# Kernel optimization log

Measured on AMD Instinct MI355X. Metric: run time of the kernel, lower is better.

The kernel has to match this reference:

```python
import jax, jax.numpy as jnp
import numpy as np
import math

N_EMBD = 1024
N_HEAD = 16
HEAD_DIM = N_EMBD // N_HEAD
SCALE = 1.0 / math.sqrt(HEAD_DIM)


def setup_inputs() -> dict:
    key = jax.random.key(0)
    ks = jax.random.split(key, 5)
    B, S = 1, 4096
    std = 0.02
    x = jax.random.normal(ks[0], (B, S, N_EMBD), dtype=jnp.float32)
    # Linear weights stored as [in, out] (transposed vs torch storage; same math)
    w_qkv = jax.random.normal(ks[1], (N_EMBD, 3 * N_EMBD), dtype=jnp.float32) * std
    b_qkv = jnp.zeros((3 * N_EMBD,), dtype=jnp.float32)
    w_out = jax.random.normal(ks[2], (N_EMBD, N_EMBD), dtype=jnp.float32) * std
    b_out = jnp.zeros((N_EMBD,), dtype=jnp.float32)
    return {"x": x, "w_qkv": w_qkv, "b_qkv": b_qkv, "w_out": w_out, "b_out": b_out}


def reference(x, w_qkv, b_qkv, w_out, b_out):
    B, S, D = x.shape
    qkv = x @ w_qkv + b_qkv                      # [B, S, 3D]
    q, k, v = jnp.split(qkv, 3, axis=-1)
    # [B, H, S, d]
    q = q.reshape(B, S, N_HEAD, HEAD_DIM).transpose(0, 2, 1, 3)
    k = k.reshape(B, S, N_HEAD, HEAD_DIM).transpose(0, 2, 1, 3)
    v = v.reshape(B, S, N_HEAD, HEAD_DIM).transpose(0, 2, 1, 3)
    scores = jnp.einsum("bhqd,bhkd->bhqk", q, k) * SCALE  # [B, H, S, S]
    causal = jnp.tril(jnp.ones((S, S), dtype=bool))
    scores = jnp.where(causal, scores, -jnp.inf)
    attn = jax.nn.softmax(scores, axis=-1)
    out = jnp.einsum("bhqk,bhkd->bhqd", attn, v)  # [B, H, S, d]
    out = out.transpose(0, 2, 1, 3).reshape(B, S, D)
    return out @ w_out + b_out
```

## Files before the change

### kernel.cpp

```cpp
#include <hip/hip_runtime.h>
#include <hip/hip_bf16.h>
#include <cstdint>

typedef __bf16 bf16x8 __attribute__((ext_vector_type(8)));
typedef float  f32x4  __attribute__((ext_vector_type(4)));

#define S_LEN 4096
#define D_EMB 1024
#define N3    3072
#define HDIM  64

__device__ __forceinline__ unsigned short f2bf(float f) {
    union { unsigned int i; float f; } v; v.f = f;
    unsigned int i = v.i;
    return (unsigned short)((i + 0x7FFFu + ((i >> 16) & 1u)) >> 16);
}

__device__ __forceinline__ void async16(const void* g, void* l) {
    __builtin_amdgcn_global_load_lds(
        (const __attribute__((address_space(1))) unsigned int*)g,
        (__attribute__((address_space(3))) unsigned int*)l,
        16, 0, 0);
}

__global__ void convert_f32_bf16(const float* __restrict__ src,
                                 unsigned short* __restrict__ dst, int n8) {
    const int i = blockIdx.x * blockDim.x + threadIdx.x;
    if (i >= n8) return;
    float4 f0 = *(const float4*)&src[i * 8];
    float4 f1 = *(const float4*)&src[i * 8 + 4];
    union { uint4 q; unsigned short s[8]; } o;
    o.s[0]=f2bf(f0.x); o.s[1]=f2bf(f0.y); o.s[2]=f2bf(f0.z); o.s[3]=f2bf(f0.w);
    o.s[4]=f2bf(f1.x); o.s[5]=f2bf(f1.y); o.s[6]=f2bf(f1.z); o.s[7]=f2bf(f1.w);
    *(uint4*)&dst[i * 8] = o.q;
}

__global__ void transpose_f32_to_bf16(const float* __restrict__ src,
                                      unsigned short* __restrict__ dst,
                                      int R, int ld, int c0) {
    __shared__ float tile[32][33];
    const int tx = threadIdx.x, ty = threadIdx.y;
    const int r0 = blockIdx.y * 32, cc0 = blockIdx.x * 32;
    for (int i = 0; i < 32; i += 8)
        tile[ty + i][tx] = src[(size_t)(r0 + ty + i) * ld + c0 + cc0 + tx];
    __syncthreads();
    for (int i = 0; i < 32; i += 8)
        dst[(size_t)(cc0 + ty + i) * R + r0 + tx] = f2bf(tile[tx][ty + i]);
}

__global__ void transpose_bf16(const unsigned short* __restrict__ src,
                               unsigned short* __restrict__ dst,
                               int R, int ld, int c0) {
    __shared__ unsigned short tile[32][33];
    const int tx = threadIdx.x, ty = threadIdx.y;
    const int r0 = blockIdx.y * 32, cc0 = blockIdx.x * 32;
    for (int i = 0; i < 32; i += 8)
        tile[ty + i][tx] = src[(size_t)(r0 + ty + i) * ld + c0 + cc0 + tx];
    __syncthreads();
    for (int i = 0; i < 32; i += 8)
        dst[(size_t)(cc0 + ty + i) * R + r0 + tx] = tile[tx][ty + i];
}

template <bool OUT_F32>
__global__ __launch_bounds__(256) void gemm_bt_bias(
    const unsigned short* __restrict__ A,
    const unsigned short* __restrict__ BT,
    const float* __restrict__ bias,
    void* __restrict__ Cp,
    int M, int N, int K)
{
    __shared__ __align__(16) unsigned short As[128 * 32];
    __shared__ __align__(16) unsigned short Bs[128 * 32];
    const int tid  = threadIdx.x;
    const int wave = tid >> 6, lane = tid & 63;
    const int q4 = lane >> 4, l16 = lane & 15;
    const int m0 = blockIdx.y * 128, n0 = blockIdx.x * 128;
    const int wm = (wave >> 1) * 64, wn = (wave & 1) * 64;

    f32x4 acc[4][4] = {};

    const int srow = wave * 32 + (lane >> 2);
    const int scol = (lane & 3) * 8;

    for (int k0 = 0; k0 < K; k0 += 32) {
        __syncthreads();
        for (int i = 0; i < 2; ++i) {
            const int r = srow + i * 16;
            async16(A  + (size_t)(m0 + r) * K + k0 + scol,
                    &As[(wave * 32 + i * 16) * 32 + lane * 8]);
            async16(BT + (size_t)(n0 + r) * K + k0 + scol,
                    &Bs[(wave * 32 + i * 16) * 32 + lane * 8]);
        }
        __syncthreads();

        bf16x8 af[4], bfr[4];
        for (int mi = 0; mi < 4; ++mi)
            af[mi] = *(const bf16x8*)&As[(wm + mi * 16 + l16) * 32 + q4 * 8];
        for (int ni = 0; ni < 4; ++ni)
            bfr[ni] = *(const bf16x8*)&Bs[(wn + ni * 16 + l16) * 32 + q4 * 8];
        for (int mi = 0; mi < 4; ++mi)
            for (int ni = 0; ni < 4; ++ni)
                acc[mi][ni] = __builtin_amdgcn_mfma_f32_16x16x32_bf16(
                    af[mi], bfr[ni], acc[mi][ni], 0, 0, 0);
    }

    for (int ni = 0; ni < 4; ++ni) {
        const int col = n0 + wn + ni * 16 + l16;
        const float bv = bias[col];
        for (int mi = 0; mi < 4; ++mi) {
            const int row = m0 + wm + mi * 16 + q4 * 4;
            for (int r = 0; r < 4; ++r) {
                const float val = acc[mi][ni][r] + bv;
                if constexpr (OUT_F32)
                    ((float*)Cp)[(size_t)(row + r) * N + col] = val;
                else
                    ((unsigned short*)Cp)[(size_t)(row + r) * N + col] = f2bf(val);
            }
        }
    }
}

#define LDP 72
__global__ __launch_bounds__(256) void attn_flash(
    const unsigned short* __restrict__ qkv,
    const unsigned short* __restrict__ Vt,
    unsigned short* __restrict__ X2)
{
    __shared__ __align__(16) unsigned short Ks[64 * LDP];
    __shared__ __align__(16) unsigned short Vs[64 * LDP];
    __shared__ __align__(16) unsigned short Ps[4 * 16 * LDP];
    const int tid  = threadIdx.x;
    const int wave = tid >> 6, lane = tid & 63;
    const int q4 = lane >> 4, l16 = lane & 15;
    const int h  = blockIdx.y;

    const int x = blockIdx.x, hg = blockIdx.y >> 2;
    int qt;
    if      (hg == 0) qt = x;
    else if (hg == 1) qt = 63 - x;
    else if (hg == 2) qt = (x + 16) & 63;
    else              qt = (47 - x) & 63;
    const int q0 = qt * 64;

    bf16x8 aq[2];
    {
        const unsigned short* qp =
            qkv + (size_t)(q0 + wave * 16 + l16) * N3 + h * HDIM + q4 * 8;
        aq[0] = *(const bf16x8*)(qp);
        aq[1] = *(const bf16x8*)(qp + 32);
    }

    float l_part[4] = {0.f, 0.f, 0.f, 0.f};
    f32x4 o[4] = {};

    const int rr = tid >> 3;
    const int cc = (tid & 7) * 8;
    const int ntile = qt + 1;

    for (int t = 0; t < ntile; ++t) {
        const int kv0 = t * 64;
        uint4 kv_a = *(const uint4*)&qkv[(size_t)(kv0 + rr)      * N3 + D_EMB + h * HDIM + cc];
        uint4 kv_b = *(const uint4*)&qkv[(size_t)(kv0 + 32 + rr) * N3 + D_EMB + h * HDIM + cc];
        uint4 vt_a = *(const uint4*)&Vt [(size_t)(h * HDIM + rr)      * S_LEN + kv0 + cc];
        uint4 vt_b = *(const uint4*)&Vt [(size_t)(h * HDIM + 32 + rr) * S_LEN + kv0 + cc];
        __syncthreads();
        *(uint4*)&Ks[rr * LDP + cc]        = kv_a;
        *(uint4*)&Ks[(32 + rr) * LDP + cc] = kv_b;
        *(uint4*)&Vs[rr * LDP + cc]        = vt_a;
        *(uint4*)&Vs[(32 + rr) * LDP + cc] = vt_b;
        __syncthreads();

        f32x4 sacc[4] = {};
        for (int kk = 0; kk < 2; ++kk)
            for (int nt = 0; nt < 4; ++nt) {
                bf16x8 b = *(const bf16x8*)&Ks[(nt * 16 + l16) * LDP + kk * 32 + q4 * 8];
                sacc[nt] = __builtin_amdgcn_mfma_f32_16x16x32_bf16(
                    aq[kk], b, sacc[nt], 0, 0, 0);
            }

        const bool lastt = (t == ntile - 1);
        for (int r = 0; r < 4; ++r) {
            const int grow = q0 + wave * 16 + q4 * 4 + r;
            for (int nt = 0; nt < 4; ++nt) {
                float e = __expf(sacc[nt][r] * 0.125f);
                if (lastt && (kv0 + nt * 16 + l16 > grow)) e = 0.f;
                l_part[r] += e;
                Ps[wave * 16 * LDP + (q4 * 4 + r) * LDP + nt * 16 + l16] = f2bf(e);
            }
        }
        __asm__ volatile("s_waitcnt lgkmcnt(0)" ::: "memory");

        for (int kk = 0; kk < 2; ++kk) {
            bf16x8 pa = *(const bf16x8*)&Ps[wave * 16 * LDP + l16 * LDP + kk * 32 + q4 * 8];
            for (int dt = 0; dt < 4; ++dt) {
                bf16x8 vb = *(const bf16x8*)&Vs[(dt * 16 + l16) * LDP + kk * 32 + q4 * 8];
                o[dt] = __builtin_amdgcn_mfma_f32_16x16x32_bf16(pa, vb, o[dt], 0, 0, 0);
            }
        }
    }

    float linv[4];
    for (int r = 0; r < 4; ++r) {
        float l = l_part[r];
        for (int off = 1; off < 16; off <<= 1)
            l += __shfl_xor(l, off, 16);
        linv[r] = 1.f / l;
    }
    for (int dt = 0; dt < 4; ++dt)
        for (int r = 0; r < 4; ++r) {
            const int row = q0 + wave * 16 + q4 * 4 + r;
            X2[(size_t)row * D_EMB + h * HDIM + dt * 16 + l16] =
                f2bf(o[dt][r] * linv[r]);
        }
}

extern "C" void kernel_launch(void* const* d_in, const int* in_sizes, int n_in,
                              void* d_out, int out_size, void* d_ws, size_t ws_size,
                              hipStream_t stream) {
    const float* x     = (const float*)d_in[0];
    const float* w_qkv = (const float*)d_in[1];
    const float* b_qkv = (const float*)d_in[2];
    const float* w_out = (const float*)d_in[3];
    const float* b_out = (const float*)d_in[4];
    float* out = (float*)d_out;

    char* ws = (char*)d_ws;
    unsigned short* qkv   = (unsigned short*)(ws);
    unsigned short* wqkvT = (unsigned short*)(ws + 25165824);
    unsigned short* woutT = (unsigned short*)(ws + 31457280);
    unsigned short* Vt    = (unsigned short*)(ws + 33554432);
    unsigned short* X2    = (unsigned short*)(ws + 41943040);
    unsigned short* Xb    = X2;

    convert_f32_bf16<<<(4096 * 1024 / 8 + 255) / 256, 256, 0, stream>>>(
        x, Xb, 4096 * 1024 / 8);

    transpose_f32_to_bf16<<<dim3(3072 / 32, 1024 / 32), dim3(32, 8), 0, stream>>>(
        w_qkv, wqkvT, 1024, 3072, 0);
    transpose_f32_to_bf16<<<dim3(1024 / 32, 1024 / 32), dim3(32, 8), 0, stream>>>(
        w_out, woutT, 1024, 1024, 0);

    gemm_bt_bias<false><<<dim3(3072 / 128, 4096 / 128), 256, 0, stream>>>(
        Xb, wqkvT, b_qkv, qkv, 4096, 3072, 1024);

    transpose_bf16<<<dim3(1024 / 32, 4096 / 32), dim3(32, 8), 0, stream>>>(
        qkv, Vt, 4096, 3072, 2048);

    attn_flash<<<dim3(64, 16), 256, 0, stream>>>(qkv, Vt, X2);

    gemm_bt_bias<true><<<dim3(1024 / 128, 4096 / 128), 256, 0, stream>>>(
        X2, woutT, b_out, out, 4096, 1024, 1024);
}
```

Measured before the change: 248.4 us.

## Fuse V transpose into QKV GEMM epilogue, shrink out-proj tile, cheapen softmax

The QKV GEMM now writes the V block directly in transposed layout from its epilogue, so the separate transpose kernel launch and its extra pass over V are gone. The output projection uses a 64-row M tile, doubling the block count to improve occupancy on a small grid. Attention switches to exp2 with a folded scale, splits the causal mask into a separate last-tile branch, and converts to bf16 by truncation instead of round-to-nearest, which adds a small precision risk. The fused V epilogue writes 4-element strided stores, which may be less coalesced than the old transpose.

```diff
diff --git a/kernel.cpp b/kernel.cpp
--- a/kernel.cpp
+++ b/kernel.cpp
@@ -48,66 +48,73 @@
         dst[(size_t)(cc0 + ty + i) * R + r0 + tx] = f2bf(tile[tx][ty + i]);
 }
 
-__global__ void transpose_bf16(const unsigned short* __restrict__ src,
-                               unsigned short* __restrict__ dst,
-                               int R, int ld, int c0) {
-    __shared__ unsigned short tile[32][33];
-    const int tx = threadIdx.x, ty = threadIdx.y;
-    const int r0 = blockIdx.y * 32, cc0 = blockIdx.x * 32;
-    for (int i = 0; i < 32; i += 8)
-        tile[ty + i][tx] = src[(size_t)(r0 + ty + i) * ld + c0 + cc0 + tx];
-    __syncthreads();
-    for (int i = 0; i < 32; i += 8)
-        dst[(size_t)(cc0 + ty + i) * R + r0 + tx] = tile[tx][ty + i];
-}
-
-template <bool OUT_F32>
+template <int MI, bool OUT_F32, bool FUSE_VT>
 __global__ __launch_bounds__(256) void gemm_bt_bias(
     const unsigned short* __restrict__ A,
     const unsigned short* __restrict__ BT,
     const float* __restrict__ bias,
     void* __restrict__ Cp,
+    unsigned short* __restrict__ Vt,
     int M, int N, int K)
 {
-    __shared__ __align__(16) unsigned short As[128 * 32];
+    constexpr int MTILE = MI * 32;
+    constexpr int LA = MI / 2;
+    __shared__ __align__(16) unsigned short As[MTILE * 32];
     __shared__ __align__(16) unsigned short Bs[128 * 32];
     const int tid  = threadIdx.x;
     const int wave = tid >> 6, lane = tid & 63;
     const int q4 = lane >> 4, l16 = lane & 15;
-    const int m0 = blockIdx.y * 128, n0 = blockIdx.x * 128;
-    const int wm = (wave >> 1) * 64, wn = (wave & 1) * 64;
-
-    f32x4 acc[4][4] = {};
-
-    const int srow = wave * 32 + (lane >> 2);
+    const int m0 = blockIdx.y * MTILE, n0 = blockIdx.x * 128;
+    const int wm = (wave >> 1) * (MI * 16), wn = (wave & 1) * 64;
+
+    f32x4 acc[MI][4] = {};
+
+    const int lrow = lane >> 2;
     const int scol = (lane & 3) * 8;
 
     for (int k0 = 0; k0 < K; k0 += 32) {
         __syncthreads();
         for (int i = 0; i < 2; ++i) {
-            const int r = srow + i * 16;
-            async16(A  + (size_t)(m0 + r) * K + k0 + scol,
-                    &As[(wave * 32 + i * 16) * 32 + lane * 8]);
+            const int r = wave * 32 + i * 16 + lrow;
             async16(BT + (size_t)(n0 + r) * K + k0 + scol,
                     &Bs[(wave * 32 + i * 16) * 32 + lane * 8]);
         }
-        __syncthreads();
-
-        bf16x8 af[4], bfr[4];
-        for (int mi = 0; mi < 4; ++mi)
+        for (int i = 0; i < LA; ++i) {
+            const int r = wave * (16 * LA) + i * 16 + lrow;
+            async16(A + (size_t)(m0 + r) * K + k0 + scol,
+                    &As[(wave * (16 * LA) + i * 16) * 32 + lane * 8]);
+        }
+        __syncthreads();
+
+        bf16x8 af[MI], bfr[4];
+        for (int mi = 0; mi < MI; ++mi)
             af[mi] = *(const bf16x8*)&As[(wm + mi * 16 + l16) * 32 + q4 * 8];
         for (int ni = 0; ni < 4; ++ni)
             bfr[ni] = *(const bf16x8*)&Bs[(wn + ni * 16 + l16) * 32 + q4 * 8];
-        for (int mi = 0; mi < 4; ++mi)
+        for (int mi = 0; mi < MI; ++mi)
             for (int ni = 0; ni < 4; ++ni)
                 acc[mi][ni] = __builtin_amdgcn_mfma_f32_16x16x32_bf16(
                     af[mi], bfr[ni], acc[mi][ni], 0, 0, 0);
     }
 
+    if (FUSE_VT && n0 >= 2048) {
+        for (int ni = 0; ni < 4; ++ni) {
+            const int col = n0 + wn + ni * 16 + l16;
+            const float bv = bias[col];
+            const int vrow = col - 2048;
+            for (int mi = 0; mi < MI; ++mi) {
+                const int row = m0 + wm + mi * 16 + q4 * 4;
+                union { uint2 u; unsigned short s[4]; } pk;
+                for (int r = 0; r < 4; ++r) pk.s[r] = f2bf(acc[mi][ni][r] + bv);
+                *(uint2*)&Vt[(size_t)vrow * S_LEN + row] = pk.u;
+            }
+        }
+        return;
+    }
     for (int ni = 0; ni < 4; ++ni) {
         const int col = n0 + wn + ni * 16 + l16;
         const float bv = bias[col];
-        for (int mi = 0; mi < 4; ++mi) {
+        for (int mi = 0; mi < MI; ++mi) {
             const int row = m0 + wm + mi * 16 + q4 * 4;
             for (int r = 0; r < 4; ++r) {
                 const float val = acc[mi][ni][r] + bv;
@@ -121,6 +128,8 @@
 }
 
 #define LDP 72
+#define EXP2_SCALE 0.180336884f
+
 __global__ __launch_bounds__(256) void attn_flash(
     const unsigned short* __restrict__ qkv,
     const unsigned short* __restrict__ Vt,
@@ -155,9 +164,9 @@
 
     const int rr = tid >> 3;
     const int cc = (tid & 7) * 8;
-    const int ntile = qt + 1;
-
-    for (int t = 0; t < ntile; ++t) {
+    unsigned short* Pw = &Ps[wave * 16 * LDP];
+
+    for (int t = 0; t <= qt; ++t) {
         const int kv0 = t * 64;
         uint4 kv_a = *(const uint4*)&qkv[(size_t)(kv0 + rr)      * N3 + D_EMB + h * HDIM + cc];
         uint4 kv_b = *(const uint4*)&qkv[(size_t)(kv0 + 32 + rr) * N3 + D_EMB + h * HDIM + cc];
@@ -178,20 +187,33 @@
                     aq[kk], b, sacc[nt], 0, 0, 0);
             }
 
-        const bool lastt = (t == ntile - 1);
-        for (int r = 0; r < 4; ++r) {
-            const int grow = q0 + wave * 16 + q4 * 4 + r;
-            for (int nt = 0; nt < 4; ++nt) {
-                float e = __expf(sacc[nt][r] * 0.125f);
-                if (lastt && (kv0 + nt * 16 + l16 > grow)) e = 0.f;
-                l_part[r] += e;
-                Ps[wave * 16 * LDP + (q4 * 4 + r) * LDP + nt * 16 + l16] = f2bf(e);
+        if (t < qt) {
+            for (int r = 0; r < 4; ++r) {
+                const int prow = (q4 * 4 + r) * LDP;
+                for (int nt = 0; nt < 4; ++nt) {
+                    float e = exp2f(sacc[nt][r] * EXP2_SCALE);
+                    l_part[r] += e;
+                    Pw[prow + nt * 16 + l16] =
+                        (unsigned short)(__float_as_uint(e) >> 16);
+                }
+            }
+        } else {
+            for (int r = 0; r < 4; ++r) {
+                const int grow = q0 + wave * 16 + q4 * 4 + r;
+                const int prow = (q4 * 4 + r) * LDP;
+                for (int nt = 0; nt < 4; ++nt) {
+                    float e = exp2f(sacc[nt][r] * EXP2_SCALE);
+                    if (kv0 + nt * 16 + l16 > grow) e = 0.f;
+                    l_part[r] += e;
+                    Pw[prow + nt * 16 + l16] =
+                        (unsigned short)(__float_as_uint(e) >> 16);
+                }
             }
         }
         __asm__ volatile("s_waitcnt lgkmcnt(0)" ::: "memory");
 
         for (int kk = 0; kk < 2; ++kk) {
-            bf16x8 pa = *(const bf16x8*)&Ps[wave * 16 * LDP + l16 * LDP + kk * 32 + q4 * 8];
+            bf16x8 pa = *(const bf16x8*)&Pw[l16 * LDP + kk * 32 + q4 * 8];
             for (int dt = 0; dt < 4; ++dt) {
                 bf16x8 vb = *(const bf16x8*)&Vs[(dt * 16 + l16) * LDP + kk * 32 + q4 * 8];
                 o[dt] = __builtin_amdgcn_mfma_f32_16x16x32_bf16(pa, vb, o[dt], 0, 0, 0);
@@ -240,14 +262,11 @@
     transpose_f32_to_bf16<<<dim3(1024 / 32, 1024 / 32), dim3(32, 8), 0, stream>>>(
         w_out, woutT, 1024, 1024, 0);
 
-    gemm_bt_bias<false><<<dim3(3072 / 128, 4096 / 128), 256, 0, stream>>>(
-        Xb, wqkvT, b_qkv, qkv, 4096, 3072, 1024);
-
-    transpose_bf16<<<dim3(1024 / 32, 4096 / 32), dim3(32, 8), 0, stream>>>(
-        qkv, Vt, 4096, 3072, 2048);
+    gemm_bt_bias<4, false, true><<<dim3(3072 / 128, 4096 / 128), 256, 0, stream>>>(
+        Xb, wqkvT, b_qkv, qkv, Vt, 4096, 3072, 1024);
 
     attn_flash<<<dim3(64, 16), 256, 0, stream>>>(qkv, Vt, X2);
 
-    gemm_bt_bias<true><<<dim3(1024 / 128, 4096 / 128), 256, 0, stream>>>(
-        X2, woutT, b_out, out, 4096, 1024, 1024);
-}
+    gemm_bt_bias<2, true, false><<<dim3(1024 / 128, 4096 / 64), 256, 0, stream>>>(
+        X2, woutT, b_out, out, nullptr, 4096, 1024, 1024);
+}
```

After: 251.6 us. Within noise of the previous version (+1.3%).
